# Kernel optimization log

Hardware: AMD Instinct MI355X
Metric: run time of the kernel (lower is better)

## Reference

```python
import jax, jax.numpy as jnp
import numpy as np

B, N, D, H = 2, 2048, 1024, 16
HD = D // H

def setup_inputs() -> dict:
    key = jax.random.key(0)
    ks = jax.random.split(key, 5)
    s_in = 1.0 / np.sqrt(D)
    x = jax.random.normal(ks[0], (B, N, D), dtype=jnp.float32)
    W_qkv = jax.random.uniform(ks[1], (3 * D, D), minval=-s_in, maxval=s_in, dtype=jnp.float32)
    b_qkv = jax.random.uniform(ks[2], (3 * D,), minval=-s_in, maxval=s_in, dtype=jnp.float32)
    W_out = jax.random.uniform(ks[3], (D, D), minval=-s_in, maxval=s_in, dtype=jnp.float32)
    b_out = jax.random.uniform(ks[4], (D,), minval=-s_in, maxval=s_in, dtype=jnp.float32)
    return {"x": x, "W_qkv": W_qkv, "b_qkv": b_qkv, "W_out": W_out, "b_out": b_out}

def reference(x, W_qkv, b_qkv, W_out, b_out):
    scale = HD ** (-0.5)
    qkv = x @ W_qkv.T + b_qkv                       # [B,N,3D]
    q, k, v = jnp.split(qkv, 3, axis=-1)
    # [B,N,D] -> [B,H,N,HD]
    def heads(t):
        return t.reshape(B, N, H, HD).transpose(0, 2, 1, 3)
    q, k, v = heads(q), heads(k), heads(v)
    attn = jnp.einsum('bhqd,bhkd->bhqk', q, k) * scale   # [B,H,N,N]
    causal = jnp.tril(jnp.ones((N, N), dtype=bool))
    attn = jnp.where(causal, attn, -jnp.inf)
    attn = jax.nn.softmax(attn, axis=-1)
    out = jnp.einsum('bhqk,bhkd->bhqd', attn, v)         # [B,H,N,HD]
    out = out.transpose(0, 2, 1, 3).reshape(B, N, D)
    return out @ W_out.T + b_out
```

## Files before the change

### kernel.cpp

```cpp
#include <hip/hip_runtime.h>
#include <hip/hip_bf16.h>

#define Bdim 2
#define Nseq 2048
#define Dmod 1024
#define Hn   16
#define HDim 64

#define XN  (Bdim * Nseq * Dmod)
#define WQN (3 * Dmod * Dmod)
#define WON (Dmod * Dmod)

typedef __attribute__((ext_vector_type(8))) __bf16 bf16x8;
typedef __attribute__((ext_vector_type(4))) __bf16 bf16x4;
typedef __attribute__((ext_vector_type(4))) float  floatx4;

__device__ __forceinline__ floatx4 mfma16(bf16x8 a, bf16x8 b, floatx4 c) {
    return __builtin_amdgcn_mfma_f32_16x16x32_bf16(a, b, c, 0, 0, 0);
}

__device__ __forceinline__ float exp2v(float x) {
    return __builtin_amdgcn_exp2f(x);
}

__device__ __forceinline__ void async_copy16(__bf16* l, const __bf16* g) {
    __builtin_amdgcn_global_load_lds(
        (const __attribute__((address_space(1))) void*)g,
        (__attribute__((address_space(3))) void*)l,
        16, 0, 0);
}

__global__ __launch_bounds__(256) void convert_kernel(
    const float* __restrict__ x, const float* __restrict__ wq,
    const float* __restrict__ wo,
    __bf16* __restrict__ xb, __bf16* __restrict__ wqb, __bf16* __restrict__ wob)
{
    int i = (blockIdx.x * 256 + threadIdx.x) * 4;
    const float* src;
    __bf16* dst;
    int off;
    if (i < XN)            { src = x;  dst = xb;  off = i; }
    else if (i < XN + WQN) { src = wq; dst = wqb; off = i - XN; }
    else                   { src = wo; dst = wob; off = i - XN - WQN; }
    float4 v = *(const float4*)(src + off);
    bf16x4 o;
    o.x = (__bf16)v.x; o.y = (__bf16)v.y; o.z = (__bf16)v.z; o.w = (__bf16)v.w;
    *(bf16x4*)(dst + off) = o;
}

__global__ __launch_bounds__(256) void qkv_kernel(
    const __bf16* __restrict__ x, const __bf16* __restrict__ Wq,
    const float* __restrict__ bq,
    __bf16* __restrict__ qb, __bf16* __restrict__ kb, __bf16* __restrict__ vt)
{
    __shared__ __align__(16) __bf16 ldsA[128 * 32];
    __shared__ __align__(16) __bf16 ldsB[128 * 32];

    const int tid  = threadIdx.x;
    const int lane = tid & 63, l16 = lane & 15, quad = lane >> 4;
    const int wiw  = tid >> 6;
    const int wm   = wiw & 1, wn = wiw >> 1;

    const int bm = blockIdx.x & 31;
    const int bn = blockIdx.x >> 5;
    const int m0 = bm * 128, n0 = bn * 128;

    const int srow = tid >> 2;
    const int scol = (tid & 3) * 8;

    floatx4 z = {0.f, 0.f, 0.f, 0.f};
    floatx4 acc[4][4];
    #pragma unroll
    for (int mt = 0; mt < 4; ++mt)
        #pragma unroll
        for (int nt = 0; nt < 4; ++nt) acc[mt][nt] = z;

    const __bf16* ga = x  + (size_t)m0 * Dmod;
    const __bf16* gb = Wq + (size_t)n0 * Dmod;

    for (int k0 = 0; k0 < Dmod; k0 += 32) {
        async_copy16(&ldsA[srow * 32 + scol],        ga + (size_t)srow * Dmod + k0 + scol);
        async_copy16(&ldsA[(64 + srow) * 32 + scol], ga + (size_t)(64 + srow) * Dmod + k0 + scol);
        async_copy16(&ldsB[srow * 32 + scol],        gb + (size_t)srow * Dmod + k0 + scol);
        async_copy16(&ldsB[(64 + srow) * 32 + scol], gb + (size_t)(64 + srow) * Dmod + k0 + scol);
        __syncthreads();

        bf16x8 af[4], bfr[4];
        #pragma unroll
        for (int mt = 0; mt < 4; ++mt)
            af[mt] = *(const bf16x8*)&ldsA[(wm * 64 + mt * 16 + l16) * 32 + quad * 8];
        #pragma unroll
        for (int nt = 0; nt < 4; ++nt)
            bfr[nt] = *(const bf16x8*)&ldsB[(wn * 64 + nt * 16 + l16) * 32 + quad * 8];
        #pragma unroll
        for (int mt = 0; mt < 4; ++mt)
            #pragma unroll
            for (int nt = 0; nt < 4; ++nt)
                acc[mt][nt] = mfma16(af[mt], bfr[nt], acc[mt][nt]);
        __syncthreads();
    }

    const int nb    = n0 + wn * 64;
    const int which = nb >> 10;
    const int h     = (nb & 1023) >> 6;
    const int mw    = m0 + wm * 64;
    const int bi    = mw >> 11;
    const int pos0  = mw & (Nseq - 1);

    #pragma unroll
    for (int nt = 0; nt < 4; ++nt) {
        float bias = bq[nb + nt * 16 + l16];
        int hd = nt * 16 + l16;
        #pragma unroll
        for (int mt = 0; mt < 4; ++mt)
            #pragma unroll
            for (int i = 0; i < 4; ++i) {
                int pos = pos0 + mt * 16 + quad * 4 + i;
                __bf16 v = (__bf16)(acc[mt][nt][i] + bias);
                if (which == 0)
                    qb[((bi * Hn + h) * Nseq + pos) * HDim + hd] = v;
                else if (which == 1)
                    kb[((bi * Hn + h) * Nseq + pos) * HDim + hd] = v;
                else
                    vt[((bi * Hn + h) * HDim + hd) * Nseq + pos] = v;
            }
    }
}

__global__ __launch_bounds__(256, 4) void attn_kernel(
    const __bf16* __restrict__ qbuf, const __bf16* __restrict__ kbuf,
    const __bf16* __restrict__ vtbuf, __bf16* __restrict__ aout)
{
    __shared__ __align__(16) __bf16 ldsK[64 * 64];
    __shared__ __align__(16) __bf16 ldsV[64 * 64];
    __shared__ __align__(16) __bf16 ldsP[4][16 * 72];

    const int tid  = threadIdx.x;
    const int wiw  = tid >> 6;
    const int lane = tid & 63, l16 = lane & 15, quad = lane >> 4;
    const int b    = blockIdx.x;
    const int bh   = b & 31;
    const int qb   = 31 - (b >> 5);
    const int q0   = qb * 64 + wiw * 16;

    const __bf16* qs = qbuf  + bh * Nseq * HDim;
    const __bf16* ks = kbuf  + bh * Nseq * HDim;
    const __bf16* vs = vtbuf + bh * HDim * Nseq;

    const int srow = tid >> 3;
    const int scol = (tid & 7) * 8;

    bf16x8 qf0 = *(const bf16x8*)(qs + (q0 + l16) * HDim + quad * 8);
    bf16x8 qf1 = *(const bf16x8*)(qs + (q0 + l16) * HDim + 32 + quad * 8);

    floatx4 z = {0.f, 0.f, 0.f, 0.f};
    floatx4 o[4];
    #pragma unroll
    for (int s = 0; s < 4; ++s) o[s] = z;
    float m_i = -1e30f, l_i = 0.f;

    const float C   = 0.125f * 1.44269504f;
    const int   nkt = qb + 1;
    __bf16* myp = ldsP[wiw];

    for (int kt = 0; kt < nkt; ++kt) {
        const int k0 = kt * 64;
        const bool last = (kt == nkt - 1);

        async_copy16(&ldsK[srow * 64 + scol],
                     ks + (size_t)(k0 + srow) * HDim + scol);
        async_copy16(&ldsK[(srow + 32) * 64 + scol],
                     ks + (size_t)(k0 + srow + 32) * HDim + scol);
        async_copy16(&ldsV[srow * 64 + scol],
                     vs + (size_t)srow * Nseq + k0 + scol);
        async_copy16(&ldsV[(srow + 32) * 64 + scol],
                     vs + (size_t)(srow + 32) * Nseq + k0 + scol);
        __syncthreads();

        floatx4 st[4];
        #pragma unroll
        for (int t = 0; t < 4; ++t) {
            bf16x8 kf0 = *(const bf16x8*)&ldsK[(t * 16 + l16) * 64 + quad * 8];
            bf16x8 kf1 = *(const bf16x8*)&ldsK[(t * 16 + l16) * 64 + 32 + quad * 8];
            st[t] = mfma16(kf0, qf0, z);
            st[t] = mfma16(kf1, qf1, st[t]);
        }

        float a[16];
        #pragma unroll
        for (int t = 0; t < 4; ++t)
            #pragma unroll
            for (int i = 0; i < 4; ++i) {
                float v = st[t][i] * C;
                if (last) {
                    int kidx = t * 16 + quad * 4 + i;
                    v = (kidx <= wiw * 16 + l16) ? v : -1e30f;
                }
                a[t * 4 + i] = v;
            }

        float mx = a[0];
        #pragma unroll
        for (int j = 1; j < 16; ++j) mx = fmaxf(mx, a[j]);
        mx = fmaxf(mx, __shfl_xor(mx, 16));
        mx = fmaxf(mx, __shfl_xor(mx, 32));

        float mn    = fmaxf(m_i, mx);
        float alpha = exp2v(m_i - mn);

        float p[16], rs = 0.f;
        #pragma unroll
        for (int j = 0; j < 16; ++j) { p[j] = exp2v(a[j] - mn); rs += p[j]; }
        rs += __shfl_xor(rs, 16);
        rs += __shfl_xor(rs, 32);
        l_i = l_i * alpha + rs;
        m_i = mn;

        #pragma unroll
        for (int s = 0; s < 4; ++s)
            #pragma unroll
            for (int i = 0; i < 4; ++i) o[s][i] *= alpha;

        #pragma unroll
        for (int t = 0; t < 4; ++t) {
            bf16x4 pk;
            pk.x = (__bf16)p[t * 4 + 0]; pk.y = (__bf16)p[t * 4 + 1];
            pk.z = (__bf16)p[t * 4 + 2]; pk.w = (__bf16)p[t * 4 + 3];
            *(bf16x4*)(myp + l16 * 72 + t * 16 + quad * 4) = pk;
        }
        asm volatile("s_waitcnt lgkmcnt(0)" ::: "memory");
        bf16x8 pf0 = *(const bf16x8*)(myp + l16 * 72 + quad * 8);
        bf16x8 pf1 = *(const bf16x8*)(myp + l16 * 72 + 32 + quad * 8);

        #pragma unroll
        for (int s = 0; s < 4; ++s) {
            bf16x8 vf0 = *(const bf16x8*)&ldsV[(s * 16 + l16) * 64 + quad * 8];
            bf16x8 vf1 = *(const bf16x8*)&ldsV[(s * 16 + l16) * 64 + 32 + quad * 8];
            o[s] = mfma16(vf0, pf0, o[s]);
            o[s] = mfma16(vf1, pf1, o[s]);
        }
        __syncthreads();
    }

    const float inv = 1.0f / l_i;
    const int bi = bh >> 4, h = bh & 15;
    #pragma unroll
    for (int s = 0; s < 4; ++s) {
        bf16x4 ov;
        ov.x = (__bf16)(o[s][0] * inv); ov.y = (__bf16)(o[s][1] * inv);
        ov.z = (__bf16)(o[s][2] * inv); ov.w = (__bf16)(o[s][3] * inv);
        *(bf16x4*)(aout + ((size_t)(bi * Nseq + q0 + l16)) * Dmod
                   + h * 64 + s * 16 + quad * 4) = ov;
    }
}

__global__ __launch_bounds__(256) void proj_kernel(
    const __bf16* __restrict__ ao, const __bf16* __restrict__ Wo,
    const float* __restrict__ bo, float* __restrict__ out)
{
    __shared__ __align__(16) __bf16 ldsA[128 * 32];
    __shared__ __align__(16) __bf16 ldsB[128 * 32];

    const int tid  = threadIdx.x;
    const int lane = tid & 63, l16 = lane & 15, quad = lane >> 4;
    const int wiw  = tid >> 6;
    const int wm   = wiw & 1, wn = wiw >> 1;

    const int bm = blockIdx.x & 31;
    const int bn = blockIdx.x >> 5;
    const int m0 = bm * 128, n0 = bn * 128;

    const int srow = tid >> 2;
    const int scol = (tid & 3) * 8;

    floatx4 z = {0.f, 0.f, 0.f, 0.f};
    floatx4 acc[4][4];
    #pragma unroll
    for (int mt = 0; mt < 4; ++mt)
        #pragma unroll
        for (int nt = 0; nt < 4; ++nt) acc[mt][nt] = z;

    const __bf16* ga = ao + (size_t)m0 * Dmod;
    const __bf16* gb = Wo + (size_t)n0 * Dmod;

    for (int k0 = 0; k0 < Dmod; k0 += 32) {
        async_copy16(&ldsA[srow * 32 + scol],        ga + (size_t)srow * Dmod + k0 + scol);
        async_copy16(&ldsA[(64 + srow) * 32 + scol], ga + (size_t)(64 + srow) * Dmod + k0 + scol);
        async_copy16(&ldsB[srow * 32 + scol],        gb + (size_t)srow * Dmod + k0 + scol);
        async_copy16(&ldsB[(64 + srow) * 32 + scol], gb + (size_t)(64 + srow) * Dmod + k0 + scol);
        __syncthreads();

        bf16x8 af[4], bfr[4];
        #pragma unroll
        for (int mt = 0; mt < 4; ++mt)
            af[mt] = *(const bf16x8*)&ldsA[(wm * 64 + mt * 16 + l16) * 32 + quad * 8];
        #pragma unroll
        for (int nt = 0; nt < 4; ++nt)
            bfr[nt] = *(const bf16x8*)&ldsB[(wn * 64 + nt * 16 + l16) * 32 + quad * 8];
        #pragma unroll
        for (int mt = 0; mt < 4; ++mt)
            #pragma unroll
            for (int nt = 0; nt < 4; ++nt)
                acc[mt][nt] = mfma16(af[mt], bfr[nt], acc[mt][nt]);
        __syncthreads();
    }

    const int nb = n0 + wn * 64;
    const int mw = m0 + wm * 64;
    #pragma unroll
    for (int nt = 0; nt < 4; ++nt) {
        float bias = bo[nb + nt * 16 + l16];
        #pragma unroll
        for (int mt = 0; mt < 4; ++mt)
            #pragma unroll
            for (int i = 0; i < 4; ++i) {
                int m = mw + mt * 16 + quad * 4 + i;
                out[(size_t)m * Dmod + nb + nt * 16 + l16] = acc[mt][nt][i] + bias;
            }
    }
}

extern "C" void kernel_launch(void* const* d_in, const int* in_sizes, int n_in,
                              void* d_out, int out_size, void* d_ws, size_t ws_size,
                              hipStream_t stream) {
    const float* x  = (const float*)d_in[0];
    const float* Wq = (const float*)d_in[1];
    const float* bq = (const float*)d_in[2];
    const float* Wo = (const float*)d_in[3];
    const float* bo = (const float*)d_in[4];
    float* out = (float*)d_out;

    __bf16* ws  = (__bf16*)d_ws;
    __bf16* xb  = ws;
    __bf16* wqb = ws + (size_t)XN;
    __bf16* wob = wqb + (size_t)WQN;
    __bf16* qb  = wob + (size_t)WON;
    const size_t SZ = (size_t)Bdim * Hn * Nseq * HDim;
    __bf16* kb  = qb + SZ;
    __bf16* vt  = kb + SZ;
    __bf16* ao  = vt + SZ;

    convert_kernel<<<dim3(8192), dim3(256), 0, stream>>>(x, Wq, Wo, xb, wqb, wob);
    qkv_kernel<<<dim3(768), dim3(256), 0, stream>>>(xb, wqb, bq, qb, kb, vt);
    attn_kernel<<<dim3(1024), dim3(256), 0, stream>>>(qb, kb, vt, ao);
    proj_kernel<<<dim3(256), dim3(256), 0, stream>>>(ao, wob, bo, out);
}
```

Measured before the change: 201.0 us.

## Register-prefetch next K/V tile and XOR-swizzle LDS layout in attention

Replaces the synchronous async_copy16 loads of each K/V tile with a register double-buffer: the next tile is loaded into registers while the current one is computed, then written to LDS at the top of the next iteration. The LDS layout gets an XOR swizzle on 16-byte chunks to avoid bank conflicts on the row-strided fragment reads. Max and sum reductions become trees to shorten dependency chains. The prefetch costs extra VGPRs, which may reduce occupancy under the 4-wave launch bound.

Measured after the change: 188.2 us. 1.07x faster.

```diff
diff --git a/kernel.cpp b/kernel.cpp
--- a/kernel.cpp
+++ b/kernel.cpp
@@ -140,15 +140,18 @@
     const int lane = tid & 63, l16 = lane & 15, quad = lane >> 4;
     const int b    = blockIdx.x;
     const int bh   = b & 31;
-    const int qb   = 31 - (b >> 5);
-    const int q0   = qb * 64 + wiw * 16;
+    const int qblk = 31 - (b >> 5);
+    const int q0   = qblk * 64 + wiw * 16;
 
     const __bf16* qs = qbuf  + bh * Nseq * HDim;
     const __bf16* ks = kbuf  + bh * Nseq * HDim;
     const __bf16* vs = vtbuf + bh * HDim * Nseq;
 
-    const int srow = tid >> 3;
-    const int scol = (tid & 7) * 8;
+    const int sr  = tid >> 3;
+    const int sb  = tid & 7;
+    const int swr = (sb ^ (sr & 7)) * 8;
+    const int wk0 = sr * 64 + swr;
+    const int wk1 = (sr + 32) * 64 + swr;
 
     bf16x8 qf0 = *(const bf16x8*)(qs + (q0 + l16) * HDim + quad * 8);
     bf16x8 qf1 = *(const bf16x8*)(qs + (q0 + l16) * HDim + 32 + quad * 8);
@@ -160,28 +163,39 @@
     float m_i = -1e30f, l_i = 0.f;
 
     const float C   = 0.125f * 1.44269504f;
-    const int   nkt = qb + 1;
+    const int   nkt = qblk + 1;
     __bf16* myp = ldsP[wiw];
+    const int swz = l16 & 7;
+
+    float4 rk0 = *(const float4*)(ks + (size_t)sr * HDim + sb * 8);
+    float4 rk1 = *(const float4*)(ks + (size_t)(sr + 32) * HDim + sb * 8);
+    float4 rv0 = *(const float4*)(vs + (size_t)sr * Nseq + sb * 8);
+    float4 rv1 = *(const float4*)(vs + (size_t)(sr + 32) * Nseq + sb * 8);
 
     for (int kt = 0; kt < nkt; ++kt) {
-        const int k0 = kt * 64;
+        float4 nk0 = {}, nk1 = {}, nv0 = {}, nv1 = {};
+        if (kt + 1 < nkt) {
+            const int k0n = (kt + 1) * 64;
+            nk0 = *(const float4*)(ks + (size_t)(k0n + sr) * HDim + sb * 8);
+            nk1 = *(const float4*)(ks + (size_t)(k0n + sr + 32) * HDim + sb * 8);
+            nv0 = *(const float4*)(vs + (size_t)sr * Nseq + k0n + sb * 8);
+            nv1 = *(const float4*)(vs + (size_t)(sr + 32) * Nseq + k0n + sb * 8);
+        }
+
+        *(float4*)&ldsK[wk0] = rk0;
+        *(float4*)&ldsK[wk1] = rk1;
+        *(float4*)&ldsV[wk0] = rv0;
+        *(float4*)&ldsV[wk1] = rv1;
+        __syncthreads();
+
         const bool last = (kt == nkt - 1);
 
-        async_copy16(&ldsK[srow * 64 + scol],
-                     ks + (size_t)(k0 + srow) * HDim + scol);
-        async_copy16(&ldsK[(srow + 32) * 64 + scol],
-                     ks + (size_t)(k0 + srow + 32) * HDim + scol);
-        async_copy16(&ldsV[srow * 64 + scol],
-                     vs + (size_t)srow * Nseq + k0 + scol);
-        async_copy16(&ldsV[(srow + 32) * 64 + scol],
-                     vs + (size_t)(srow + 32) * Nseq + k0 + scol);
-        __syncthreads();
-
         floatx4 st[4];
         #pragma unroll
         for (int t = 0; t < 4; ++t) {
-            bf16x8 kf0 = *(const bf16x8*)&ldsK[(t * 16 + l16) * 64 + quad * 8];
-            bf16x8 kf1 = *(const bf16x8*)&ldsK[(t * 16 + l16) * 64 + 32 + quad * 8];
+            const __bf16* kr = &ldsK[(t * 16 + l16) * 64];
+            bf16x8 kf0 = *(const bf16x8*)(kr + ((quad ^ swz) * 8));
+            bf16x8 kf1 = *(const bf16x8*)(kr + (((quad + 4) ^ swz) * 8));
             st[t] = mfma16(kf0, qf0, z);
             st[t] = mfma16(kf1, qf1, st[t]);
         }
@@ -199,18 +213,25 @@
                 a[t * 4 + i] = v;
             }
 
-        float mx = a[0];
-        #pragma unroll
-        for (int j = 1; j < 16; ++j) mx = fmaxf(mx, a[j]);
+        float mA = fmaxf(fmaxf(a[0], a[1]),  fmaxf(a[2], a[3]));
+        float mB = fmaxf(fmaxf(a[4], a[5]),  fmaxf(a[6], a[7]));
+        float mC = fmaxf(fmaxf(a[8], a[9]),  fmaxf(a[10], a[11]));
+        float mD = fmaxf(fmaxf(a[12], a[13]), fmaxf(a[14], a[15]));
+        float mx = fmaxf(fmaxf(mA, mB), fmaxf(mC, mD));
         mx = fmaxf(mx, __shfl_xor(mx, 16));
         mx = fmaxf(mx, __shfl_xor(mx, 32));
 
         float mn    = fmaxf(m_i, mx);
         float alpha = exp2v(m_i - mn);
 
-        float p[16], rs = 0.f;
-        #pragma unroll
-        for (int j = 0; j < 16; ++j) { p[j] = exp2v(a[j] - mn); rs += p[j]; }
+        float p[16];
+        #pragma unroll
+        for (int j = 0; j < 16; ++j) p[j] = exp2v(a[j] - mn);
+        float sA = (p[0] + p[1]) + (p[2] + p[3]);
+        float sB = (p[4] + p[5]) + (p[6] + p[7]);
+        float sC = (p[8] + p[9]) + (p[10] + p[11]);
+        float sD = (p[12] + p[13]) + (p[14] + p[15]);
+        float rs = (sA + sB) + (sC + sD);
         rs += __shfl_xor(rs, 16);
         rs += __shfl_xor(rs, 32);
         l_i = l_i * alpha + rs;
@@ -234,12 +255,15 @@
 
         #pragma unroll
         for (int s = 0; s < 4; ++s) {
-            bf16x8 vf0 = *(const bf16x8*)&ldsV[(s * 16 + l16) * 64 + quad * 8];
-            bf16x8 vf1 = *(const bf16x8*)&ldsV[(s * 16 + l16) * 64 + 32 + quad * 8];
+            const __bf16* vr = &ldsV[(s * 16 + l16) * 64];
+            bf16x8 vf0 = *(const bf16x8*)(vr + ((quad ^ swz) * 8));
+            bf16x8 vf1 = *(const bf16x8*)(vr + (((quad + 4) ^ swz) * 8));
             o[s] = mfma16(vf0, pf0, o[s]);
             o[s] = mfma16(vf1, pf1, o[s]);
         }
         __syncthreads();
+
+        rk0 = nk0; rk1 = nk1; rv0 = nv0; rv1 = nv1;
     }
 
     const float inv = 1.0f / l_i;
```
